# Optimization experiments

Hardware: AMD Instinct MI355X
Metric: run time of the kernel (lower is better)

The kernel has to match this reference:

```python
import jax, jax.numpy as jnp
import numpy as np
import math

B, Q, C, H, L, P = 8, 900, 256, 8, 4, 4
D = C // H  # head_dim = 32
SPATIAL = np.array([[100, 100], [50, 50], [25, 25], [13, 13]], dtype=np.int64)
AREAS = SPATIAL[:, 0] * SPATIAL[:, 1]
STARTS = np.concatenate([[0], np.cumsum(AREAS)[:-1]]).astype(np.int64)
S = int(AREAS.sum())  # 13294


def _xavier(k, i, o, scale=1.0):
    return jax.random.normal(k, (i, o), jnp.float32) * scale * (2.0 / (i + o)) ** 0.5


def setup_inputs() -> dict:
    key = jax.random.key(0)
    ks = jax.random.split(key, 16)
    inp = {}
    inp['query'] = jax.random.normal(ks[0], (B, Q, C), jnp.float32)
    inp['reference_points'] = jax.random.uniform(ks[1], (B, Q, L, 2), jnp.float32)
    inp['input_flatten'] = jax.random.normal(ks[2], (B, S, C), jnp.float32)
    inp['object_shape'] = jax.random.uniform(ks[3], (B, Q, 2), jnp.float32) * 0.3 + 0.02
    inp['input_spatial_shapes'] = jnp.asarray(SPATIAL)
    inp['input_level_start_index'] = jnp.asarray(STARTS)
    # learned parameters (torch zero-inits offset/attn weights; use small random for a nontrivial baseline)
    inp['w_q'] = _xavier(ks[4], C, C); inp['b_q'] = jnp.zeros((C,), jnp.float32)
    inp['w_v'] = _xavier(ks[5], C, C); inp['b_v'] = jnp.zeros((C,), jnp.float32)
    inp['w_o'] = _xavier(ks[6], C, C); inp['b_o'] = jnp.zeros((C,), jnp.float32)
    inp['w_off1'] = _xavier(ks[7], C + 2, C); inp['b_off1'] = jnp.zeros((C,), jnp.float32)
    inp['w_off2'] = _xavier(ks[8], C, H * L * P * 2, scale=0.05)
    inp['b_off2'] = jax.random.normal(ks[9], (H * L * P * 2,), jnp.float32) * 0.02
    inp['w_ax'] = _xavier(ks[10], C, H * L * P, scale=0.1); inp['b_ax'] = jnp.zeros((H * L * P,), jnp.float32)
    inp['w_ay'] = _xavier(ks[11], C, H * L * P, scale=0.1); inp['b_ay'] = jnp.zeros((H * L * P,), jnp.float32)
    # spectral basis per original init: head h uses freq pi*(h+1)/H over arange(D)
    freq = (np.arange(1, H + 1, dtype=np.float32)[:, None] * math.pi / H) * np.arange(D, dtype=np.float32)[None, :]
    inp['basis_x'] = jnp.asarray(np.cos(freq), jnp.float32)
    inp['basis_y'] = jnp.asarray(np.sin(freq), jnp.float32)
    return inp


def _bilinear_sample(v, locs):
    """v: (B,S,H,D); locs: (B,Q,H,L,P,2) in [0,1]. grid_sample semantics: align_corners=False, zeros padding.
    Returns (B,Q,H,L,P,D)."""
    levels = []
    for lvl in range(L):
        Hl, Wl = int(SPATIAL[lvl, 0]), int(SPATIAL[lvl, 1])
        start = int(STARTS[lvl])
        v_l = v[:, start:start + Hl * Wl]  # (B, Hl*Wl, H, D)
        loc = locs[:, :, :, lvl]  # (B,Q,H,P,2)
        # align_corners=False: pixel coord = loc * size - 0.5
        x = loc[..., 0] * Wl - 0.5
        y = loc[..., 1] * Hl - 0.5
        x0 = jnp.floor(x); y0 = jnp.floor(y)
        fx = x - x0; fy = y - y0
        x0i = x0.astype(jnp.int32); y0i = y0.astype(jnp.int32)
        acc = jnp.zeros((B, Q, H, P, D), jnp.float32)
        corners = [(0, 0, (1 - fx) * (1 - fy)), (1, 0, fx * (1 - fy)),
                   (0, 1, (1 - fx) * fy), (1, 1, fx * fy)]
        for dx, dy, w in corners:
            xi = x0i + dx; yi = y0i + dy
            valid = (xi >= 0) & (xi < Wl) & (yi >= 0) & (yi < Hl)
            idx = jnp.clip(yi, 0, Hl - 1) * Wl + jnp.clip(xi, 0, Wl - 1)  # (B,Q,H,P)
            idx_t = idx.transpose(0, 1, 3, 2).reshape(B, Q * P, H)[..., None]  # (B,Q*P,H,1)
            g = jnp.take_along_axis(v_l, idx_t, axis=1)  # (B,Q*P,H,D)
            g = g.reshape(B, Q, P, H, D).transpose(0, 1, 3, 2, 4)  # (B,Q,H,P,D)
            acc = acc + g * (w * valid.astype(jnp.float32))[..., None]
        levels.append(acc)
    return jnp.stack(levels, axis=3)  # (B,Q,H,L,P,D)


def reference(query, reference_points, input_flatten, input_spatial_shapes, input_level_start_index,
              object_shape, w_q, b_q, w_v, b_v, w_o, b_o, w_off1, b_off1, w_off2, b_off2,
              w_ax, b_ax, w_ay, b_ay, basis_x, basis_y):
    q = query @ w_q + b_q  # (B,Q,C)
    v = (input_flatten @ w_v + b_v).reshape(B, S, H, D)
    q_shape = jnp.concatenate([q, object_shape], axis=-1)  # (B,Q,C+2)
    hid = jax.nn.relu(q_shape @ w_off1 + b_off1)
    offsets = (hid @ w_off2 + b_off2).reshape(B, Q, H, L, P, 2)
    offsets = offsets * object_shape[:, :, None, None, None, :]
    ref = reference_points[:, :, None, :, None, :]  # (B,Q,1,L,1,2)
    locs = jnp.clip(ref + offsets, 0.0, 1.0)  # (B,Q,H,L,P,2)
    q_heads = q.reshape(B, Q, H, D)
    spec = jnp.einsum('bqhd,hd->bqh', q_heads, basis_x) * jnp.einsum('bqhd,hd->bqh', q_heads, basis_y)
    attn_x = (q @ w_ax + b_ax).reshape(B, Q, H, L, P)
    attn_y = (q @ w_ay + b_ay).reshape(B, Q, H, L, P)
    attn = attn_x * attn_y + spec[..., None, None]
    attn = jax.nn.softmax(attn.reshape(B, Q, H, L * P), axis=-1).reshape(B, Q, H, L, P)
    sampled = _bilinear_sample(v, locs)  # (B,Q,H,L,P,D)
    out = (sampled * attn[..., None]).sum(axis=(3, 4)).reshape(B, Q, C)
    return out @ w_o + b_o  # dropout is identity in eval
```

## Files before the change

kernel.cpp:

```cpp
#include <hip/hip_runtime.h>
#include <hip/hip_bf16.h>
#include <math.h>

constexpr int B_ = 8, Q_ = 900;
constexpr int S_ = 13294;
constexpr int BQ = 7200;
constexpr int BS = 106352;
constexpr int NVB = 831;

typedef __bf16 bf16x8 __attribute__((ext_vector_type(8)));
typedef float  f32x4  __attribute__((ext_vector_type(4)));

#define WAITLGKM0 asm volatile("s_waitcnt lgkmcnt(0)" ::: "memory")
#define SCHEDB    __builtin_amdgcn_sched_barrier(0)
#define BAR       __builtin_amdgcn_s_barrier()
#define CFENCE    asm volatile("" ::: "memory")

__device__ __forceinline__ void load_lds16(const void* g, void* lds) {
    __builtin_amdgcn_global_load_lds(
        (const __attribute__((address_space(1))) void*)g,
        (__attribute__((address_space(3))) void*)lds, 16, 0, 0);
}

__global__ __launch_bounds__(256)
void transpose_all(const float* __restrict__ wv, const float* __restrict__ wo,
                   const float* __restrict__ woff1, const float* __restrict__ woff2,
                   const float* __restrict__ wax, const float* __restrict__ way,
                   __bf16* __restrict__ tv, __bf16* __restrict__ to_,
                   __bf16* __restrict__ toff2, __bf16* __restrict__ tcat)
{
    const int bi = blockIdx.x;
    __shared__ float tile[32][33];
    const int tx = threadIdx.x & 31, ty = threadIdx.x >> 5;

    const float* src; __bf16* dst; int k0, n0, scol, sN = 256;
    if (bi < 192) {
        const int wid = bi >> 6, t = bi & 63;
        k0 = (t & 7) * 32; n0 = (t >> 3) * 32; scol = n0;
        if      (wid == 0) { src = wv;    dst = tv;    }
        else if (wid == 1) { src = wo;    dst = to_;   }
        else               { src = woff2; dst = toff2; }
    } else {
        const int t = bi - 192;
        k0 = (t & 7) * 32; n0 = (t >> 3) * 32;
        dst = tcat;
        if      (n0 < 128) { src = wax;   scol = n0;       sN = 128; }
        else if (n0 < 256) { src = way;   scol = n0 - 128; sN = 128; }
        else               { src = woff1; scol = n0 - 256; sN = 256; }
    }

    #pragma unroll
    for (int i = 0; i < 4; ++i)
        tile[ty + 8 * i][tx] = src[(size_t)(k0 + ty + 8 * i) * sN + scol + tx];
    __syncthreads();
    #pragma unroll
    for (int i = 0; i < 4; ++i)
        dst[(size_t)(n0 + ty + 8 * i) * 256 + k0 + tx] = (__bf16)tile[tx][ty + 8 * i];
}

__global__ __launch_bounds__(256)
void combine2(const __bf16* __restrict__ tcat, const float* __restrict__ wq,
              const float* __restrict__ bq, const float* __restrict__ bax,
              const float* __restrict__ bay, const float* __restrict__ boff1,
              __bf16* __restrict__ wcomb, float* __restrict__ bcomb)
{
    const int bi = blockIdx.x;
    if (bi >= 8) {
        const int n = (bi - 8) * 256 + threadIdx.x;
        float acc = (n < 128) ? bax[n] : (n < 256 ? bay[n - 128] : boff1[n - 256]);
        const __bf16* row = tcat + (size_t)n * 256;
        #pragma unroll 4
        for (int c8 = 0; c8 < 32; ++c8) {
            const bf16x8 rv = *(const bf16x8*)(row + c8 * 8);
            #pragma unroll
            for (int j = 0; j < 8; ++j) acc += bq[c8 * 8 + j] * (float)rv[j];
        }
        bcomb[n] = acc;
        return;
    }

    const int wid  = (bi << 2) + (threadIdx.x >> 6);
    const int lane = threadIdx.x & 63;
    const int n0 = (wid >> 2) * 64, k0 = (wid & 3) * 64;
    const int l15 = lane & 15, l4 = lane >> 4;

    f32x4 acc[4][4] = {};
    #pragma unroll
    for (int s = 0; s < 8; ++s) {
        const int c0 = s * 32 + l4 * 8;
        bf16x8 am[4], bm[4];
        #pragma unroll
        for (int mi = 0; mi < 4; ++mi)
            am[mi] = *(const bf16x8*)(tcat + (size_t)(n0 + mi * 16 + l15) * 256 + c0);
        #pragma unroll
        for (int ni = 0; ni < 4; ++ni) {
            const float* wr_ = wq + (size_t)(k0 + ni * 16 + l15) * 256 + c0;
            const float4 f0 = ((const float4*)wr_)[0];
            const float4 f1 = ((const float4*)wr_)[1];
            bm[ni][0] = (__bf16)f0.x; bm[ni][1] = (__bf16)f0.y;
            bm[ni][2] = (__bf16)f0.z; bm[ni][3] = (__bf16)f0.w;
            bm[ni][4] = (__bf16)f1.x; bm[ni][5] = (__bf16)f1.y;
            bm[ni][6] = (__bf16)f1.z; bm[ni][7] = (__bf16)f1.w;
        }
        #pragma unroll
        for (int mi = 0; mi < 4; ++mi)
            #pragma unroll
            for (int ni = 0; ni < 4; ++ni)
                acc[mi][ni] = __builtin_amdgcn_mfma_f32_16x16x32_bf16(
                    am[mi], bm[ni], acc[mi][ni], 0, 0, 0);
    }
    #pragma unroll
    for (int mi = 0; mi < 4; ++mi)
        #pragma unroll
        for (int rr = 0; rr < 4; ++rr) {
            const int n = n0 + mi * 16 + l4 * 4 + rr;
            #pragma unroll
            for (int ni = 0; ni < 4; ++ni)
                wcomb[(size_t)n * 256 + k0 + ni * 16 + l15] = (__bf16)acc[mi][ni][rr];
        }
}

__global__ __launch_bounds__(512)
void main_fused(const float* __restrict__ x_in, const __bf16* __restrict__ wt_v,
                const float* __restrict__ b_v, __bf16* __restrict__ v_bf,
                const float* __restrict__ query, const __bf16* __restrict__ wcomb,
                const float* __restrict__ bcomb, const float* __restrict__ objs,
                const float* __restrict__ wex, float* __restrict__ axyhid)
{
    __shared__ float4 AsbV[2][512];
    __shared__ float4 BsbV[3][1024];
    char* const Asb_b = (char*)AsbV;
    char* const Bsb_b = (char*)BsbV;

    const int bid  = blockIdx.x;
    const bool isV = (bid < NVB);
    const int qb   = bid - NVB;
    const int colhalf = isV ? 0 : (qb & 1);

    const float*  A    = isV ? x_in : query;
    const __bf16* Wt   = isV ? wt_v : (wcomb + (size_t)colhalf * 256 * 256);
    const float*  bias = isV ? b_v  : (bcomb + colhalf * 256);
    const int     M    = isV ? BS   : BQ;
    const int     row0 = isV ? bid * 128 : (qb >> 1) * 128;

    const int tid  = threadIdx.x;
    const int wave = tid >> 6, lane = tid & 63;
    const int wr = wave >> 2, wc = wave & 3;
    const int l15 = lane & 15, l4 = lane >> 4;

    const int st_row = tid >> 2, st_kq = tid & 3;
    const int gr_cl  = min(row0 + st_row, M - 1);
    const float* Abase = A + (size_t)gr_cl * 256 + st_kq * 8;
    const int a_wo = st_row * 64 + ((st_kq ^ ((st_row >> 1) & 3)) * 16);

    int a_off[4], b_off[4];
    #pragma unroll
    for (int mi = 0; mi < 4; ++mi) {
        const int r = wr * 64 + mi * 16 + l15;
        a_off[mi] = r * 64 + (l4 ^ ((r >> 1) & 3)) * 16;
    }
    #pragma unroll
    for (int ni = 0; ni < 4; ++ni) {
        const int c = wc * 64 + ni * 16 + l15;
        b_off[ni] = c * 64 + (l4 ^ ((c >> 1) & 3)) * 16;
    }

    const __bf16* bsrc[2];
    #pragma unroll
    for (int i = 0; i < 2; ++i) {
        const int c   = (wave * 2 + i) * 64 + lane;
        const int col = c >> 2, kcp = c & 3;
        const int kc  = kcp ^ ((col >> 1) & 3);
        bsrc[i] = Wt + (size_t)col * 256 + kc * 8;
    }

    auto issueB = [&](int kt, int bbuf) {
        #pragma unroll
        for (int i = 0; i < 2; ++i)
            load_lds16(bsrc[i] + kt * 32, Bsb_b + bbuf * 16384 + (wave * 2 + i) * 1024);
    };
    auto loadA = [&](int kt, float4* g) {
        const float* ga = Abase + kt * 32;
        g[0] = ((const float4*)ga)[0];
        g[1] = ((const float4*)ga)[1];
    };
    auto writeA = [&](int abuf, const float4* g) {
        bf16x8 c0;
        c0[0] = (__bf16)g[0].x; c0[1] = (__bf16)g[0].y; c0[2] = (__bf16)g[0].z; c0[3] = (__bf16)g[0].w;
        c0[4] = (__bf16)g[1].x; c0[5] = (__bf16)g[1].y; c0[6] = (__bf16)g[1].z; c0[7] = (__bf16)g[1].w;
        *(bf16x8*)(Asb_b + abuf * 8192 + a_wo) = c0;
    };

    f32x4 acc[4][4] = {};
    float4 g[2][2];

    issueB(0, 0);
    loadA(0, g[0]);
    issueB(1, 1);
    loadA(1, g[1]);
    writeA(0, g[0]);
    WAITLGKM0; BAR; CFENCE; SCHEDB;

    #pragma unroll
    for (int u = 0; u < 8; ++u) {
        if (u + 2 <= 7) {
            loadA(u + 2, g[u & 1]);
            issueB(u + 2, (u + 2) % 3);
        }

        const char* Ab = Asb_b + (u & 1) * 8192;
        const char* Bb = Bsb_b + (u % 3) * 16384;
        bf16x8 a[4], b[4];
        #pragma unroll
        for (int mi = 0; mi < 4; ++mi) a[mi] = *(const bf16x8*)(Ab + a_off[mi]);
        #pragma unroll
        for (int ni = 0; ni < 4; ++ni) b[ni] = *(const bf16x8*)(Bb + b_off[ni]);

        #pragma unroll
        for (int mi = 0; mi < 4; ++mi)
            #pragma unroll
            for (int ni = 0; ni < 4; ++ni)
                acc[mi][ni] = __builtin_amdgcn_mfma_f32_16x16x32_bf16(
                    a[mi], b[ni], acc[mi][ni], 0, 0, 0);

        if (u + 1 <= 7) {
            writeA((u + 1) & 1, g[(u + 1) & 1]);
            WAITLGKM0; BAR; CFENCE; SCHEDB;
        }
    }

    float bb[4];
    #pragma unroll
    for (int ni = 0; ni < 4; ++ni) bb[ni] = bias[wc * 64 + ni * 16 + l15];

    if (isV) {
        #pragma unroll
        for (int mi = 0; mi < 4; ++mi)
            #pragma unroll
            for (int rr = 0; rr < 4; ++rr) {
                const int row = row0 + wr * 64 + mi * 16 + l4 * 4 + rr;
                if (row >= M) continue;
                #pragma unroll
                for (int ni = 0; ni < 4; ++ni)
                    v_bf[(size_t)row * 256 + wc * 64 + ni * 16 + l15] =
                        (__bf16)(acc[mi][ni][rr] + bb[ni]);
            }
    } else {
        float we0[4], we1[4];
        #pragma unroll
        for (int ni = 0; ni < 4; ++ni) {
            const int c = wc * 64 + ni * 16 + l15;
            we0[ni] = colhalf ? wex[c]       : 0.f;
            we1[ni] = colhalf ? wex[256 + c] : 0.f;
        }
        #pragma unroll
        for (int mi = 0; mi < 4; ++mi)
            #pragma unroll
            for (int rr = 0; rr < 4; ++rr) {
                const int row = row0 + wr * 64 + mi * 16 + l4 * 4 + rr;
                if (row >= M) continue;
                const float e0 = objs[(size_t)row * 2];
                const float e1 = objs[(size_t)row * 2 + 1];
                #pragma unroll
                for (int ni = 0; ni < 4; ++ni) {
                    const int c = wc * 64 + ni * 16 + l15;
                    float v = acc[mi][ni][rr] + bb[ni];
                    if (colhalf) {
                        v += e0 * we0[ni] + e1 * we1[ni];
                        v = fmaxf(v, 0.f);
                    }
                    axyhid[(size_t)row * 512 + colhalf * 256 + c] = v;
                }
            }
    }
}

template<bool OUTBF16>
__global__ __launch_bounds__(256)
void gemm_dp(const float* __restrict__ A, const __bf16* __restrict__ Wt,
             const float* __restrict__ bias, void* __restrict__ outp,
             int M, int N, int LDA)
{
    __shared__ float4 AsbV[2][512];
    __shared__ float4 BsbV[3][512];
    char* const Asb_b = (char*)AsbV;
    char* const Bsb_b = (char*)BsbV;

    const int tid  = threadIdx.x;
    const int wave = tid >> 6, lane = tid & 63;
    const int wr = wave >> 1, wc = wave & 1;
    const int row0 = blockIdx.y * 128, col0 = blockIdx.x * 128;
    const int l15 = lane & 15, l4 = lane >> 4;

    const int st_row = tid >> 1, st_kh = tid & 1;
    const int gr_cl  = min(row0 + st_row, M - 1);
    const float* Abase = A + (size_t)gr_cl * LDA + st_kh * 16;
    const int asw   = (st_row >> 1) & 3;
    const int a_wo0 = st_row * 64 + ((st_kh * 2)     ^ asw) * 16;
    const int a_wo1 = st_row * 64 + ((st_kh * 2 + 1) ^ asw) * 16;

    int a_off[4], b_off[4];
    #pragma unroll
    for (int mi = 0; mi < 4; ++mi) {
        const int r   = wr * 64 + mi * 16 + l15;
        a_off[mi] = r * 64 + (l4 ^ ((r >> 1) & 3)) * 16;
    }
    #pragma unroll
    for (int ni = 0; ni < 4; ++ni) {
        const int c   = wc * 64 + ni * 16 + l15;
        b_off[ni] = c * 64 + (l4 ^ ((c >> 1) & 3)) * 16;
    }

    const __bf16* bsrc[2];
    #pragma unroll
    for (int i = 0; i < 2; ++i) {
        const int c   = (wave * 2 + i) * 64 + lane;
        const int col = c >> 2, kcp = c & 3;
        const int kc  = kcp ^ ((col >> 1) & 3);
        bsrc[i] = Wt + (size_t)(col0 + col) * 256 + kc * 8;
    }

    auto issueB = [&](int kt, int bbuf) {
        #pragma unroll
        for (int i = 0; i < 2; ++i)
            load_lds16(bsrc[i] + kt * 32, Bsb_b + bbuf * 8192 + (wave * 2 + i) * 1024);
    };
    auto loadA = [&](int kt, float4* g) {
        const float* ga = Abase + kt * 32;
        g[0] = ((const float4*)ga)[0];
        g[1] = ((const float4*)ga)[1];
        g[2] = ((const float4*)ga)[2];
        g[3] = ((const float4*)ga)[3];
    };
    auto writeA = [&](int abuf, const float4* g) {
        bf16x8 c0, c1;
        c0[0] = (__bf16)g[0].x; c0[1] = (__bf16)g[0].y; c0[2] = (__bf16)g[0].z; c0[3] = (__bf16)g[0].w;
        c0[4] = (__bf16)g[1].x; c0[5] = (__bf16)g[1].y; c0[6] = (__bf16)g[1].z; c0[7] = (__bf16)g[1].w;
        c1[0] = (__bf16)g[2].x; c1[1] = (__bf16)g[2].y; c1[2] = (__bf16)g[2].z; c1[3] = (__bf16)g[2].w;
        c1[4] = (__bf16)g[3].x; c1[5] = (__bf16)g[3].y; c1[6] = (__bf16)g[3].z; c1[7] = (__bf16)g[3].w;
        *(bf16x8*)(Asb_b + abuf * 8192 + a_wo0) = c0;
        *(bf16x8*)(Asb_b + abuf * 8192 + a_wo1) = c1;
    };

    f32x4 acc[4][4] = {};
    float4 g[2][4];

    issueB(0, 0);
    loadA(0, g[0]);
    issueB(1, 1);
    loadA(1, g[1]);
    writeA(0, g[0]);
    WAITLGKM0; BAR; CFENCE; SCHEDB;

    #pragma unroll
    for (int u = 0; u < 8; ++u) {
        if (u + 2 <= 7) {
            loadA(u + 2, g[u & 1]);
            issueB(u + 2, (u + 2) % 3);
        }

        const char* Ab = Asb_b + (u & 1) * 8192;
        const char* Bb = Bsb_b + (u % 3) * 8192;
        bf16x8 a[4], b[4];
        #pragma unroll
        for (int mi = 0; mi < 4; ++mi) a[mi] = *(const bf16x8*)(Ab + a_off[mi]);
        #pragma unroll
        for (int ni = 0; ni < 4; ++ni) b[ni] = *(const bf16x8*)(Bb + b_off[ni]);

        #pragma unroll
        for (int mi = 0; mi < 4; ++mi)
            #pragma unroll
            for (int ni = 0; ni < 4; ++ni)
                acc[mi][ni] = __builtin_amdgcn_mfma_f32_16x16x32_bf16(
                    a[mi], b[ni], acc[mi][ni], 0, 0, 0);

        if (u + 1 <= 7) {
            writeA((u + 1) & 1, g[(u + 1) & 1]);
            WAITLGKM0; BAR; CFENCE; SCHEDB;
        }
    }

    float bb[4];
    #pragma unroll
    for (int ni = 0; ni < 4; ++ni) bb[ni] = bias[col0 + wc * 64 + ni * 16 + l15];
    #pragma unroll
    for (int mi = 0; mi < 4; ++mi) {
        #pragma unroll
        for (int rr = 0; rr < 4; ++rr) {
            const int row = row0 + wr * 64 + mi * 16 + l4 * 4 + rr;
            if (row >= M) continue;
            #pragma unroll
            for (int ni = 0; ni < 4; ++ni) {
                const float v = acc[mi][ni][rr] + bb[ni];
                const int colb = col0 + wc * 64 + ni * 16 + l15;
                if (OUTBF16) ((__bf16*)outp)[(size_t)row * N + colb] = (__bf16)v;
                else         ((float*)outp)[(size_t)row * N + colb]  = v;
            }
        }
    }
}

__global__ __launch_bounds__(256)
void attn_sample_kernel(const float* __restrict__ axyhid,
                        const float* __restrict__ refp, const float* __restrict__ objs,
                        const float* __restrict__ off, const __bf16* __restrict__ v,
                        float* __restrict__ agg)
{
    const int bq = blockIdx.x;
    const int b  = bq / Q_;
    const int tid = threadIdx.x;

    __shared__ float sm[128];
    __shared__ float sa[128];
    __shared__ float sl[256];

    if (tid < 128)
        sm[tid] = axyhid[(size_t)bq * 512 + tid] * axyhid[(size_t)bq * 512 + 128 + tid];
    __syncthreads();

    if (tid < 128) {
        const int hh = tid >> 4;
        float mx = -1e30f;
        #pragma unroll
        for (int i = 0; i < 16; ++i) mx = fmaxf(mx, sm[hh * 16 + i]);
        float s = 0.f;
        #pragma unroll
        for (int i = 0; i < 16; ++i) s += __expf(sm[hh * 16 + i] - mx);
        sa[tid] = __expf(sm[tid] - mx) / s;

        const int l = (tid >> 2) & 3;
        const float os0 = objs[(size_t)bq * 2], os1 = objs[(size_t)bq * 2 + 1];
        const float r0 = refp[((size_t)bq * 4 + l) * 2];
        const float r1 = refp[((size_t)bq * 4 + l) * 2 + 1];
        const float o0 = off[(size_t)bq * 256 + tid * 2]     * os0;
        const float o1 = off[(size_t)bq * 256 + tid * 2 + 1] * os1;
        sl[tid * 2]     = fminf(fmaxf(r0 + o0, 0.f), 1.f);
        sl[tid * 2 + 1] = fminf(fmaxf(r1 + o1, 0.f), 1.f);
    }
    __syncthreads();

    const int h = tid >> 5, lane32 = tid & 31;
    const int sp = lane32 >> 2, cq = lane32 & 3;
    const int chbase = h * 32 + cq * 8;
    const __bf16* vb = v + (size_t)b * S_ * 256;

    float acc8[8] = {};

    #pragma unroll
    for (int gidx = 0; gidx < 2; ++gidx) {
        const int lp  = gidx * 8 + sp;
        const int li  = h * 16 + lp;
        const int lvl = lp >> 2;
        const int Wl = (lvl == 0) ? 100 : (lvl == 1) ? 50 : (lvl == 2) ? 25 : 13;
        const int Hl = Wl;
        const int st = (lvl == 0) ? 0 : (lvl == 1) ? 10000 : (lvl == 2) ? 12500 : 13125;

        const float a  = sa[li];
        const float lx = sl[li * 2], ly = sl[li * 2 + 1];
        const float x = lx * (float)Wl - 0.5f;
        const float y = ly * (float)Hl - 0.5f;
        const float x0f = floorf(x), y0f = floorf(y);
        const float fx = x - x0f, fy = y - y0f;
        const int x0 = (int)x0f, y0 = (int)y0f;

        #pragma unroll
        for (int c = 0; c < 4; ++c) {
            const int dx = c & 1, dy = c >> 1;
            const int xi = x0 + dx, yi = y0 + dy;
            const float wgt = (dx ? fx : 1.f - fx) * (dy ? fy : 1.f - fy);
            const bool valid = (xi >= 0) & (xi < Wl) & (yi >= 0) & (yi < Hl);
            const int idx = min(max(yi, 0), Hl - 1) * Wl + min(max(xi, 0), Wl - 1);
            const float wa = valid ? a * wgt : 0.f;
            const bf16x8 gv = *(const bf16x8*)(vb + (size_t)(st + idx) * 256 + chbase);
            #pragma unroll
            for (int j = 0; j < 8; ++j) acc8[j] += wa * (float)gv[j];
        }
    }

    #pragma unroll
    for (int m = 4; m <= 16; m <<= 1)
        #pragma unroll
        for (int j = 0; j < 8; ++j)
            acc8[j] += __shfl_xor(acc8[j], m);

    if (sp == 0) {
        #pragma unroll
        for (int j = 0; j < 8; ++j)
            agg[(size_t)bq * 256 + chbase + j] = acc8[j];
    }
}

extern "C" void kernel_launch(void* const* d_in, const int* in_sizes, int n_in,
                              void* d_out, int out_size, void* d_ws, size_t ws_size,
                              hipStream_t stream)
{
    const float* query = (const float*)d_in[0];
    const float* refp  = (const float*)d_in[1];
    const float* x_in  = (const float*)d_in[2];
    const float* objs  = (const float*)d_in[3];
    const float* w_q    = (const float*)d_in[6];
    const float* b_q    = (const float*)d_in[7];
    const float* w_v    = (const float*)d_in[8];
    const float* b_v    = (const float*)d_in[9];
    const float* w_o    = (const float*)d_in[10];
    const float* b_o    = (const float*)d_in[11];
    const float* w_off1 = (const float*)d_in[12];
    const float* b_off1 = (const float*)d_in[13];
    const float* w_off2 = (const float*)d_in[14];
    const float* b_off2 = (const float*)d_in[15];
    const float* w_ax   = (const float*)d_in[16];
    const float* b_ax   = (const float*)d_in[17];
    const float* w_ay   = (const float*)d_in[18];
    const float* b_ay   = (const float*)d_in[19];

    float* ws = (float*)d_ws;
    float* axyhid_ws = ws;
    float* off_ws    = axyhid_ws + (size_t)BQ * 512;
    float* agg_ws    = off_ws    + (size_t)BQ * 256;
    float* bcomb_ws  = agg_ws    + (size_t)BQ * 256;
    __bf16* v_bf    = (__bf16*)(bcomb_ws + 512);
    __bf16* wt_v    = v_bf    + (size_t)BS * 256;
    __bf16* wt_o    = wt_v    + 256 * 256;
    __bf16* wt_off2 = wt_o    + 256 * 256;
    __bf16* wt_cat  = wt_off2 + 256 * 256;
    __bf16* wcomb   = wt_cat  + 512 * 256;

    const dim3 blk(256);

    transpose_all<<<320, blk, 0, stream>>>(w_v, w_o, w_off1, w_off2, w_ax, w_ay,
                                           wt_v, wt_o, wt_off2, wt_cat);
    combine2<<<10, blk, 0, stream>>>(wt_cat, w_q, b_q, b_ax, b_ay, b_off1,
                                     wcomb, bcomb_ws);

    main_fused<<<NVB + 114, dim3(512), 0, stream>>>(
        x_in, wt_v, b_v, v_bf,
        query, wcomb, bcomb_ws, objs, w_off1 + 256 * 256, axyhid_ws);

    gemm_dp<false><<<dim3(2, (BQ + 127) / 128), blk, 0, stream>>>(
        axyhid_ws + 256, wt_off2, b_off2, off_ws, BQ, 256, 512);

    attn_sample_kernel<<<BQ, blk, 0, stream>>>(axyhid_ws, refp, objs, off_ws,
                                               v_bf, agg_ws);

    gemm_dp<false><<<dim3(2, (BQ + 127) / 128), blk, 0, stream>>>(
        agg_ws, wt_o, b_o, (float*)d_out, BQ, 256, 256);
}
```

Baseline: 106.6 us.

## Fuse offset GEMM, deformable sampling and output projection into one kernel

```diff
diff --git a/kernel.cpp b/kernel.cpp
--- a/kernel.cpp
+++ b/kernel.cpp
@@ -275,218 +275,195 @@
     }
 }
 
-template<bool OUTBF16>
 __global__ __launch_bounds__(256)
-void gemm_dp(const float* __restrict__ A, const __bf16* __restrict__ Wt,
-             const float* __restrict__ bias, void* __restrict__ outp,
-             int M, int N, int LDA)
+void mega_tail(const float* __restrict__ axyhid, const __bf16* __restrict__ wt_off2,
+               const float* __restrict__ b_off2, const float* __restrict__ refp,
+               const float* __restrict__ objs, const __bf16* __restrict__ v,
+               const __bf16* __restrict__ wt_o, const float* __restrict__ b_o,
+               float* __restrict__ outp)
 {
-    __shared__ float4 AsbV[2][512];
-    __shared__ float4 BsbV[3][512];
-    char* const Asb_b = (char*)AsbV;
-    char* const Bsb_b = (char*)BsbV;
-
-    const int tid  = threadIdx.x;
+    __shared__ float off_s[32][256];
+    __shared__ float sm_s[32][128];
+    __shared__ float sa_s[32][128];
+    __shared__ float sl_s[32][256];
+    __shared__ float agg_s[32][260];
+
+    const int bq0 = blockIdx.x * 32;
+    const int tid = threadIdx.x;
     const int wave = tid >> 6, lane = tid & 63;
-    const int wr = wave >> 1, wc = wave & 1;
-    const int row0 = blockIdx.y * 128, col0 = blockIdx.x * 128;
     const int l15 = lane & 15, l4 = lane >> 4;
 
-    const int st_row = tid >> 1, st_kh = tid & 1;
-    const int gr_cl  = min(row0 + st_row, M - 1);
-    const float* Abase = A + (size_t)gr_cl * LDA + st_kh * 16;
-    const int asw   = (st_row >> 1) & 3;
-    const int a_wo0 = st_row * 64 + ((st_kh * 2)     ^ asw) * 16;
-    const int a_wo1 = st_row * 64 + ((st_kh * 2 + 1) ^ asw) * 16;
-
-    int a_off[4], b_off[4];
-    #pragma unroll
-    for (int mi = 0; mi < 4; ++mi) {
-        const int r   = wr * 64 + mi * 16 + l15;
-        a_off[mi] = r * 64 + (l4 ^ ((r >> 1) & 3)) * 16;
-    }
-    #pragma unroll
-    for (int ni = 0; ni < 4; ++ni) {
-        const int c   = wc * 64 + ni * 16 + l15;
-        b_off[ni] = c * 64 + (l4 ^ ((c >> 1) & 3)) * 16;
-    }
-
-    const __bf16* bsrc[2];
-    #pragma unroll
-    for (int i = 0; i < 2; ++i) {
-        const int c   = (wave * 2 + i) * 64 + lane;
-        const int col = c >> 2, kcp = c & 3;
-        const int kc  = kcp ^ ((col >> 1) & 3);
-        bsrc[i] = Wt + (size_t)(col0 + col) * 256 + kc * 8;
-    }
-
-    auto issueB = [&](int kt, int bbuf) {
-        #pragma unroll
-        for (int i = 0; i < 2; ++i)
-            load_lds16(bsrc[i] + kt * 32, Bsb_b + bbuf * 8192 + (wave * 2 + i) * 1024);
-    };
-    auto loadA = [&](int kt, float4* g) {
-        const float* ga = Abase + kt * 32;
-        g[0] = ((const float4*)ga)[0];
-        g[1] = ((const float4*)ga)[1];
-        g[2] = ((const float4*)ga)[2];
-        g[3] = ((const float4*)ga)[3];
-    };
-    auto writeA = [&](int abuf, const float4* g) {
-        bf16x8 c0, c1;
-        c0[0] = (__bf16)g[0].x; c0[1] = (__bf16)g[0].y; c0[2] = (__bf16)g[0].z; c0[3] = (__bf16)g[0].w;
-        c0[4] = (__bf16)g[1].x; c0[5] = (__bf16)g[1].y; c0[6] = (__bf16)g[1].z; c0[7] = (__bf16)g[1].w;
-        c1[0] = (__bf16)g[2].x; c1[1] = (__bf16)g[2].y; c1[2] = (__bf16)g[2].z; c1[3] = (__bf16)g[2].w;
-        c1[4] = (__bf16)g[3].x; c1[5] = (__bf16)g[3].y; c1[6] = (__bf16)g[3].z; c1[7] = (__bf16)g[3].w;
-        *(bf16x8*)(Asb_b + abuf * 8192 + a_wo0) = c0;
-        *(bf16x8*)(Asb_b + abuf * 8192 + a_wo1) = c1;
-    };
-
-    f32x4 acc[4][4] = {};
-    float4 g[2][4];
-
-    issueB(0, 0);
-    loadA(0, g[0]);
-    issueB(1, 1);
-    loadA(1, g[1]);
-    writeA(0, g[0]);
-    WAITLGKM0; BAR; CFENCE; SCHEDB;
-
-    #pragma unroll
-    for (int u = 0; u < 8; ++u) {
-        if (u + 2 <= 7) {
-            loadA(u + 2, g[u & 1]);
-            issueB(u + 2, (u + 2) % 3);
-        }
-
-        const char* Ab = Asb_b + (u & 1) * 8192;
-        const char* Bb = Bsb_b + (u % 3) * 8192;
-        bf16x8 a[4], b[4];
-        #pragma unroll
-        for (int mi = 0; mi < 4; ++mi) a[mi] = *(const bf16x8*)(Ab + a_off[mi]);
-        #pragma unroll
-        for (int ni = 0; ni < 4; ++ni) b[ni] = *(const bf16x8*)(Bb + b_off[ni]);
-
-        #pragma unroll
-        for (int mi = 0; mi < 4; ++mi)
+    {
+        f32x4 acc[2][4] = {};
+        #pragma unroll
+        for (int kt = 0; kt < 8; ++kt) {
+            const int k0 = kt * 32 + l4 * 8;
+            bf16x8 am[2], bm[4];
+            #pragma unroll
+            for (int mi = 0; mi < 2; ++mi) {
+                const float* ap = axyhid + (size_t)(bq0 + mi * 16 + l15) * 512 + 256 + k0;
+                const float4 f0 = ((const float4*)ap)[0];
+                const float4 f1 = ((const float4*)ap)[1];
+                am[mi][0] = (__bf16)f0.x; am[mi][1] = (__bf16)f0.y;
+                am[mi][2] = (__bf16)f0.z; am[mi][3] = (__bf16)f0.w;
+                am[mi][4] = (__bf16)f1.x; am[mi][5] = (__bf16)f1.y;
+                am[mi][6] = (__bf16)f1.z; am[mi][7] = (__bf16)f1.w;
+            }
             #pragma unroll
             for (int ni = 0; ni < 4; ++ni)
-                acc[mi][ni] = __builtin_amdgcn_mfma_f32_16x16x32_bf16(
-                    a[mi], b[ni], acc[mi][ni], 0, 0, 0);
-
-        if (u + 1 <= 7) {
-            writeA((u + 1) & 1, g[(u + 1) & 1]);
-            WAITLGKM0; BAR; CFENCE; SCHEDB;
-        }
-    }
-
-    float bb[4];
-    #pragma unroll
-    for (int ni = 0; ni < 4; ++ni) bb[ni] = bias[col0 + wc * 64 + ni * 16 + l15];
-    #pragma unroll
-    for (int mi = 0; mi < 4; ++mi) {
-        #pragma unroll
-        for (int rr = 0; rr < 4; ++rr) {
-            const int row = row0 + wr * 64 + mi * 16 + l4 * 4 + rr;
-            if (row >= M) continue;
-            #pragma unroll
-            for (int ni = 0; ni < 4; ++ni) {
-                const float v = acc[mi][ni][rr] + bb[ni];
-                const int colb = col0 + wc * 64 + ni * 16 + l15;
-                if (OUTBF16) ((__bf16*)outp)[(size_t)row * N + colb] = (__bf16)v;
-                else         ((float*)outp)[(size_t)row * N + colb]  = v;
-            }
-        }
-    }
-}
-
-__global__ __launch_bounds__(256)
-void attn_sample_kernel(const float* __restrict__ axyhid,
-                        const float* __restrict__ refp, const float* __restrict__ objs,
-                        const float* __restrict__ off, const __bf16* __restrict__ v,
-                        float* __restrict__ agg)
-{
-    const int bq = blockIdx.x;
-    const int b  = bq / Q_;
-    const int tid = threadIdx.x;
-
-    __shared__ float sm[128];
-    __shared__ float sa[128];
-    __shared__ float sl[256];
-
-    if (tid < 128)
-        sm[tid] = axyhid[(size_t)bq * 512 + tid] * axyhid[(size_t)bq * 512 + 128 + tid];
+                bm[ni] = *(const bf16x8*)(wt_off2 + (size_t)(wave * 64 + ni * 16 + l15) * 256 + k0);
+            #pragma unroll
+            for (int mi = 0; mi < 2; ++mi)
+                #pragma unroll
+                for (int ni = 0; ni < 4; ++ni)
+                    acc[mi][ni] = __builtin_amdgcn_mfma_f32_16x16x32_bf16(
+                        am[mi], bm[ni], acc[mi][ni], 0, 0, 0);
+        }
+        #pragma unroll
+        for (int mi = 0; mi < 2; ++mi)
+            #pragma unroll
+            for (int rr = 0; rr < 4; ++rr) {
+                const int r = mi * 16 + l4 * 4 + rr;
+                #pragma unroll
+                for (int ni = 0; ni < 4; ++ni) {
+                    const int c = wave * 64 + ni * 16 + l15;
+                    off_s[r][c] = acc[mi][ni][rr] + b_off2[c];
+                }
+            }
+    }
     __syncthreads();
 
-    if (tid < 128) {
-        const int hh = tid >> 4;
+    #pragma unroll
+    for (int it = 0; it < 16; ++it) {
+        const int idx = it * 256 + tid;
+        const int r = idx >> 7, u = idx & 127;
+        const int bq = bq0 + r;
+        sm_s[r][u] = axyhid[(size_t)bq * 512 + u] * axyhid[(size_t)bq * 512 + 128 + u];
+    }
+    __syncthreads();
+    #pragma unroll
+    for (int it = 0; it < 16; ++it) {
+        const int idx = it * 256 + tid;
+        const int r = idx >> 7, u = idx & 127;
+        const int bq = bq0 + r;
+        const int hh = u >> 4;
         float mx = -1e30f;
         #pragma unroll
-        for (int i = 0; i < 16; ++i) mx = fmaxf(mx, sm[hh * 16 + i]);
+        for (int i = 0; i < 16; ++i) mx = fmaxf(mx, sm_s[r][hh * 16 + i]);
         float s = 0.f;
         #pragma unroll
-        for (int i = 0; i < 16; ++i) s += __expf(sm[hh * 16 + i] - mx);
-        sa[tid] = __expf(sm[tid] - mx) / s;
-
-        const int l = (tid >> 2) & 3;
+        for (int i = 0; i < 16; ++i) s += __expf(sm_s[r][hh * 16 + i] - mx);
+        sa_s[r][u] = __expf(sm_s[r][u] - mx) / s;
+
+        const int l = (u >> 2) & 3;
         const float os0 = objs[(size_t)bq * 2], os1 = objs[(size_t)bq * 2 + 1];
         const float r0 = refp[((size_t)bq * 4 + l) * 2];
         const float r1 = refp[((size_t)bq * 4 + l) * 2 + 1];
-        const float o0 = off[(size_t)bq * 256 + tid * 2]     * os0;
-        const float o1 = off[(size_t)bq * 256 + tid * 2 + 1] * os1;
-        sl[tid * 2]     = fminf(fmaxf(r0 + o0, 0.f), 1.f);
-        sl[tid * 2 + 1] = fminf(fmaxf(r1 + o1, 0.f), 1.f);
+        const float o0 = off_s[r][u * 2]     * os0;
+        const float o1 = off_s[r][u * 2 + 1] * os1;
+        sl_s[r][u * 2]     = fminf(fmaxf(r0 + o0, 0.f), 1.f);
+        sl_s[r][u * 2 + 1] = fminf(fmaxf(r1 + o1, 0.f), 1.f);
     }
     __syncthreads();
 
     const int h = tid >> 5, lane32 = tid & 31;
     const int sp = lane32 >> 2, cq = lane32 & 3;
     const int chbase = h * 32 + cq * 8;
-    const __bf16* vb = v + (size_t)b * S_ * 256;
-
-    float acc8[8] = {};
-
-    #pragma unroll
-    for (int gidx = 0; gidx < 2; ++gidx) {
-        const int lp  = gidx * 8 + sp;
-        const int li  = h * 16 + lp;
-        const int lvl = lp >> 2;
-        const int Wl = (lvl == 0) ? 100 : (lvl == 1) ? 50 : (lvl == 2) ? 25 : 13;
-        const int Hl = Wl;
-        const int st = (lvl == 0) ? 0 : (lvl == 1) ? 10000 : (lvl == 2) ? 12500 : 13125;
-
-        const float a  = sa[li];
-        const float lx = sl[li * 2], ly = sl[li * 2 + 1];
-        const float x = lx * (float)Wl - 0.5f;
-        const float y = ly * (float)Hl - 0.5f;
-        const float x0f = floorf(x), y0f = floorf(y);
-        const float fx = x - x0f, fy = y - y0f;
-        const int x0 = (int)x0f, y0 = (int)y0f;
-
-        #pragma unroll
-        for (int c = 0; c < 4; ++c) {
-            const int dx = c & 1, dy = c >> 1;
-            const int xi = x0 + dx, yi = y0 + dy;
-            const float wgt = (dx ? fx : 1.f - fx) * (dy ? fy : 1.f - fy);
-            const bool valid = (xi >= 0) & (xi < Wl) & (yi >= 0) & (yi < Hl);
-            const int idx = min(max(yi, 0), Hl - 1) * Wl + min(max(xi, 0), Wl - 1);
-            const float wa = valid ? a * wgt : 0.f;
-            const bf16x8 gv = *(const bf16x8*)(vb + (size_t)(st + idx) * 256 + chbase);
-            #pragma unroll
-            for (int j = 0; j < 8; ++j) acc8[j] += wa * (float)gv[j];
-        }
-    }
-
-    #pragma unroll
-    for (int m = 4; m <= 16; m <<= 1)
-        #pragma unroll
-        for (int j = 0; j < 8; ++j)
-            acc8[j] += __shfl_xor(acc8[j], m);
-
-    if (sp == 0) {
-        #pragma unroll
-        for (int j = 0; j < 8; ++j)
-            agg[(size_t)bq * 256 + chbase + j] = acc8[j];
+
+    auto sample_row = [&](int r, float* acc8) {
+        const int bq = bq0 + r;
+        const __bf16* vb = v + (size_t)(bq / Q_) * S_ * 256;
+        #pragma unroll
+        for (int gidx = 0; gidx < 2; ++gidx) {
+            const int lp  = gidx * 8 + sp;
+            const int li  = h * 16 + lp;
+            const int lvl = lp >> 2;
+            const int Wl = (lvl == 0) ? 100 : (lvl == 1) ? 50 : (lvl == 2) ? 25 : 13;
+            const int Hl = Wl;
+            const int st = (lvl == 0) ? 0 : (lvl == 1) ? 10000 : (lvl == 2) ? 12500 : 13125;
+
+            const float a  = sa_s[r][li];
+            const float lx = sl_s[r][li * 2], ly = sl_s[r][li * 2 + 1];
+            const float x = lx * (float)Wl - 0.5f;
+            const float y = ly * (float)Hl - 0.5f;
+            const float x0f = floorf(x), y0f = floorf(y);
+            const float fx = x - x0f, fy = y - y0f;
+            const int x0 = (int)x0f, y0 = (int)y0f;
+
+            #pragma unroll
+            for (int c = 0; c < 4; ++c) {
+                const int dx = c & 1, dy = c >> 1;
+                const int xi = x0 + dx, yi = y0 + dy;
+                const float wgt = (dx ? fx : 1.f - fx) * (dy ? fy : 1.f - fy);
+                const bool valid = (xi >= 0) & (xi < Wl) & (yi >= 0) & (yi < Hl);
+                const int idx = min(max(yi, 0), Hl - 1) * Wl + min(max(xi, 0), Wl - 1);
+                const float wa = valid ? a * wgt : 0.f;
+                const bf16x8 gv = *(const bf16x8*)(vb + (size_t)(st + idx) * 256 + chbase);
+                #pragma unroll
+                for (int j = 0; j < 8; ++j) acc8[j] += wa * (float)gv[j];
+            }
+        }
+    };
+
+    #pragma unroll 2
+    for (int r2 = 0; r2 < 32; r2 += 2) {
+        float accA[8] = {}, accB[8] = {};
+        sample_row(r2,     accA);
+        sample_row(r2 + 1, accB);
+        #pragma unroll
+        for (int m = 4; m <= 16; m <<= 1)
+            #pragma unroll
+            for (int j = 0; j < 8; ++j) {
+                accA[j] += __shfl_xor(accA[j], m);
+                accB[j] += __shfl_xor(accB[j], m);
+            }
+        if (sp == 0) {
+            #pragma unroll
+            for (int j = 0; j < 8; ++j) {
+                agg_s[r2][chbase + j]     = accA[j];
+                agg_s[r2 + 1][chbase + j] = accB[j];
+            }
+        }
+    }
+    __syncthreads();
+
+    {
+        f32x4 acc[2][4] = {};
+        #pragma unroll
+        for (int kt = 0; kt < 8; ++kt) {
+            const int k0 = kt * 32 + l4 * 8;
+            bf16x8 am[2], bm[4];
+            #pragma unroll
+            for (int mi = 0; mi < 2; ++mi) {
+                const float* ap = &agg_s[mi * 16 + l15][k0];
+                const float4 f0 = ((const float4*)ap)[0];
+                const float4 f1 = ((const float4*)ap)[1];
+                am[mi][0] = (__bf16)f0.x; am[mi][1] = (__bf16)f0.y;
+                am[mi][2] = (__bf16)f0.z; am[mi][3] = (__bf16)f0.w;
+                am[mi][4] = (__bf16)f1.x; am[mi][5] = (__bf16)f1.y;
+                am[mi][6] = (__bf16)f1.z; am[mi][7] = (__bf16)f1.w;
+            }
+            #pragma unroll
+            for (int ni = 0; ni < 4; ++ni)
+                bm[ni] = *(const bf16x8*)(wt_o + (size_t)(wave * 64 + ni * 16 + l15) * 256 + k0);
+            #pragma unroll
+            for (int mi = 0; mi < 2; ++mi)
+                #pragma unroll
+                for (int ni = 0; ni < 4; ++ni)
+                    acc[mi][ni] = __builtin_amdgcn_mfma_f32_16x16x32_bf16(
+                        am[mi], bm[ni], acc[mi][ni], 0, 0, 0);
+        }
+        #pragma unroll
+        for (int mi = 0; mi < 2; ++mi)
+            #pragma unroll
+            for (int rr = 0; rr < 4; ++rr) {
+                const int row = bq0 + mi * 16 + l4 * 4 + rr;
+                #pragma unroll
+                for (int ni = 0; ni < 4; ++ni) {
+                    const int c = wave * 64 + ni * 16 + l15;
+                    outp[(size_t)row * 256 + c] = acc[mi][ni][rr] + b_o[c];
+                }
+            }
     }
 }
 
@@ -515,9 +492,7 @@
 
     float* ws = (float*)d_ws;
     float* axyhid_ws = ws;
-    float* off_ws    = axyhid_ws + (size_t)BQ * 512;
-    float* agg_ws    = off_ws    + (size_t)BQ * 256;
-    float* bcomb_ws  = agg_ws    + (size_t)BQ * 256;
+    float* bcomb_ws  = axyhid_ws + (size_t)BQ * 512;
     __bf16* v_bf    = (__bf16*)(bcomb_ws + 512);
     __bf16* wt_v    = v_bf    + (size_t)BS * 256;
     __bf16* wt_o    = wt_v    + 256 * 256;
@@ -536,12 +511,6 @@
         x_in, wt_v, b_v, v_bf,
         query, wcomb, bcomb_ws, objs, w_off1 + 256 * 256, axyhid_ws);
 
-    gemm_dp<false><<<dim3(2, (BQ + 127) / 128), blk, 0, stream>>>(
-        axyhid_ws + 256, wt_off2, b_off2, off_ws, BQ, 256, 512);
-
-    attn_sample_kernel<<<BQ, blk, 0, stream>>>(axyhid_ws, refp, objs, off_ws,
-                                               v_bf, agg_ws);
-
-    gemm_dp<false><<<dim3(2, (BQ + 127) / 128), blk, 0, stream>>>(
-        agg_ws, wt_o, b_o, (float*)d_out, BQ, 256, 256);
+    mega_tail<<<BQ / 32, blk, 0, stream>>>(
+        axyhid_ws, wt_off2, b_off2, refp, objs, v_bf, wt_o, b_o, (float*)d_out);
 }
```

After: 115.9 us. 8.7% more time.

## Read GEMM weight operand directly from global memory instead of LDS staging

Applied to the files above, without the earlier changes.

```diff
diff --git a/kernel.cpp b/kernel.cpp
--- a/kernel.cpp
+++ b/kernel.cpp
@@ -128,9 +128,7 @@
                 const float* __restrict__ wex, float* __restrict__ axyhid)
 {
     __shared__ float4 AsbV[2][512];
-    __shared__ float4 BsbV[3][1024];
     char* const Asb_b = (char*)AsbV;
-    char* const Bsb_b = (char*)BsbV;
 
     const int bid  = blockIdx.x;
     const bool isV = (bid < NVB);
@@ -153,32 +151,18 @@
     const float* Abase = A + (size_t)gr_cl * 256 + st_kq * 8;
     const int a_wo = st_row * 64 + ((st_kq ^ ((st_row >> 1) & 3)) * 16);
 
-    int a_off[4], b_off[4];
+    int a_off[4];
     #pragma unroll
     for (int mi = 0; mi < 4; ++mi) {
         const int r = wr * 64 + mi * 16 + l15;
         a_off[mi] = r * 64 + (l4 ^ ((r >> 1) & 3)) * 16;
     }
-    #pragma unroll
-    for (int ni = 0; ni < 4; ++ni) {
-        const int c = wc * 64 + ni * 16 + l15;
-        b_off[ni] = c * 64 + (l4 ^ ((c >> 1) & 3)) * 16;
-    }
-
-    const __bf16* bsrc[2];
-    #pragma unroll
-    for (int i = 0; i < 2; ++i) {
-        const int c   = (wave * 2 + i) * 64 + lane;
-        const int col = c >> 2, kcp = c & 3;
-        const int kc  = kcp ^ ((col >> 1) & 3);
-        bsrc[i] = Wt + (size_t)col * 256 + kc * 8;
-    }
-
-    auto issueB = [&](int kt, int bbuf) {
-        #pragma unroll
-        for (int i = 0; i < 2; ++i)
-            load_lds16(bsrc[i] + kt * 32, Bsb_b + bbuf * 16384 + (wave * 2 + i) * 1024);
-    };
+
+    const __bf16* bp[4];
+    #pragma unroll
+    for (int ni = 0; ni < 4; ++ni)
+        bp[ni] = Wt + (size_t)(wc * 64 + ni * 16 + l15) * 256 + l4 * 8;
+
     auto loadA = [&](int kt, float4* g) {
         const float* ga = Abase + kt * 32;
         g[0] = ((const float4*)ga)[0];
@@ -192,29 +176,24 @@
     };
 
     f32x4 acc[4][4] = {};
-    float4 g[2][2];
-
-    issueB(0, 0);
-    loadA(0, g[0]);
-    issueB(1, 1);
-    loadA(1, g[1]);
-    writeA(0, g[0]);
-    WAITLGKM0; BAR; CFENCE; SCHEDB;
+    float4 g[2];
+
+    loadA(0, g);
+    writeA(0, g);
 
     #pragma unroll
     for (int u = 0; u < 8; ++u) {
-        if (u + 2 <= 7) {
-            loadA(u + 2, g[u & 1]);
-            issueB(u + 2, (u + 2) % 3);
-        }
+        if (u < 7) loadA(u + 1, g);
+        WAITLGKM0; BAR; CFENCE; SCHEDB;
 
         const char* Ab = Asb_b + (u & 1) * 8192;
-        const char* Bb = Bsb_b + (u % 3) * 16384;
         bf16x8 a[4], b[4];
         #pragma unroll
         for (int mi = 0; mi < 4; ++mi) a[mi] = *(const bf16x8*)(Ab + a_off[mi]);
         #pragma unroll
-        for (int ni = 0; ni < 4; ++ni) b[ni] = *(const bf16x8*)(Bb + b_off[ni]);
+        for (int ni = 0; ni < 4; ++ni) b[ni] = *(const bf16x8*)(bp[ni] + u * 32);
+
+        if (u < 7) writeA((u + 1) & 1, g);
 
         #pragma unroll
         for (int mi = 0; mi < 4; ++mi)
@@ -222,11 +201,6 @@
             for (int ni = 0; ni < 4; ++ni)
                 acc[mi][ni] = __builtin_amdgcn_mfma_f32_16x16x32_bf16(
                     a[mi], b[ni], acc[mi][ni], 0, 0, 0);
-
-        if (u + 1 <= 7) {
-            writeA((u + 1) & 1, g[(u + 1) & 1]);
-            WAITLGKM0; BAR; CFENCE; SCHEDB;
-        }
     }
 
     float bb[4];
```

After: 112.5 us. 1.06x slower.

## Merge weight transpose and combine kernels into one prep launch; add explicit vmcnt waits

Applied to the files above, without the earlier changes.

```diff
diff --git a/kernel.cpp b/kernel.cpp
--- a/kernel.cpp
+++ b/kernel.cpp
@@ -22,64 +22,58 @@
         (__attribute__((address_space(3))) void*)lds, 16, 0, 0);
 }
 
+__device__ __forceinline__ float wcat_f(const float* __restrict__ wax,
+                                        const float* __restrict__ way,
+                                        const float* __restrict__ woff1,
+                                        int c, int n)
+{
+    if (n < 128) return wax[(size_t)c * 128 + n];
+    if (n < 256) return way[(size_t)c * 128 + (n - 128)];
+    return woff1[(size_t)c * 256 + (n - 256)];
+}
+
 __global__ __launch_bounds__(256)
-void transpose_all(const float* __restrict__ wv, const float* __restrict__ wo,
-                   const float* __restrict__ woff1, const float* __restrict__ woff2,
-                   const float* __restrict__ wax, const float* __restrict__ way,
-                   __bf16* __restrict__ tv, __bf16* __restrict__ to_,
-                   __bf16* __restrict__ toff2, __bf16* __restrict__ tcat)
+void prep_all(const float* __restrict__ wv, const float* __restrict__ wo,
+              const float* __restrict__ woff2, const float* __restrict__ wq,
+              const float* __restrict__ wax, const float* __restrict__ way,
+              const float* __restrict__ woff1, const float* __restrict__ bq,
+              const float* __restrict__ bax, const float* __restrict__ bay,
+              const float* __restrict__ boff1,
+              __bf16* __restrict__ tv, __bf16* __restrict__ to_,
+              __bf16* __restrict__ toff2, __bf16* __restrict__ wcomb,
+              float* __restrict__ bcomb)
 {
     const int bi = blockIdx.x;
     __shared__ float tile[32][33];
-    const int tx = threadIdx.x & 31, ty = threadIdx.x >> 5;
-
-    const float* src; __bf16* dst; int k0, n0, scol, sN = 256;
+
     if (bi < 192) {
         const int wid = bi >> 6, t = bi & 63;
-        k0 = (t & 7) * 32; n0 = (t >> 3) * 32; scol = n0;
+        const int k0 = (t & 7) * 32, n0 = (t >> 3) * 32;
+        const int tx = threadIdx.x & 31, ty = threadIdx.x >> 5;
+        const float* src; __bf16* dst;
         if      (wid == 0) { src = wv;    dst = tv;    }
         else if (wid == 1) { src = wo;    dst = to_;   }
         else               { src = woff2; dst = toff2; }
-    } else {
-        const int t = bi - 192;
-        k0 = (t & 7) * 32; n0 = (t >> 3) * 32;
-        dst = tcat;
-        if      (n0 < 128) { src = wax;   scol = n0;       sN = 128; }
-        else if (n0 < 256) { src = way;   scol = n0 - 128; sN = 128; }
-        else               { src = woff1; scol = n0 - 256; sN = 256; }
-    }
-
-    #pragma unroll
-    for (int i = 0; i < 4; ++i)
-        tile[ty + 8 * i][tx] = src[(size_t)(k0 + ty + 8 * i) * sN + scol + tx];
-    __syncthreads();
-    #pragma unroll
-    for (int i = 0; i < 4; ++i)
-        dst[(size_t)(n0 + ty + 8 * i) * 256 + k0 + tx] = (__bf16)tile[tx][ty + 8 * i];
-}
-
-__global__ __launch_bounds__(256)
-void combine2(const __bf16* __restrict__ tcat, const float* __restrict__ wq,
-              const float* __restrict__ bq, const float* __restrict__ bax,
-              const float* __restrict__ bay, const float* __restrict__ boff1,
-              __bf16* __restrict__ wcomb, float* __restrict__ bcomb)
-{
-    const int bi = blockIdx.x;
-    if (bi >= 8) {
-        const int n = (bi - 8) * 256 + threadIdx.x;
+        #pragma unroll
+        for (int i = 0; i < 4; ++i)
+            tile[ty + 8 * i][tx] = src[(size_t)(k0 + ty + 8 * i) * 256 + n0 + tx];
+        __syncthreads();
+        #pragma unroll
+        for (int i = 0; i < 4; ++i)
+            dst[(size_t)(n0 + ty + 8 * i) * 256 + k0 + tx] = (__bf16)tile[tx][ty + 8 * i];
+        return;
+    }
+
+    if (bi >= 200) {
+        const int n = (bi - 200) * 256 + threadIdx.x;
         float acc = (n < 128) ? bax[n] : (n < 256 ? bay[n - 128] : boff1[n - 256]);
-        const __bf16* row = tcat + (size_t)n * 256;
-        #pragma unroll 4
-        for (int c8 = 0; c8 < 32; ++c8) {
-            const bf16x8 rv = *(const bf16x8*)(row + c8 * 8);
-            #pragma unroll
-            for (int j = 0; j < 8; ++j) acc += bq[c8 * 8 + j] * (float)rv[j];
-        }
+        for (int c = 0; c < 256; ++c)
+            acc += bq[c] * (float)(__bf16)wcat_f(wax, way, woff1, c, n);
         bcomb[n] = acc;
         return;
     }
 
-    const int wid  = (bi << 2) + (threadIdx.x >> 6);
+    const int wid  = ((bi - 192) << 2) + (threadIdx.x >> 6);
     const int lane = threadIdx.x & 63;
     const int n0 = (wid >> 2) * 64, k0 = (wid & 3) * 64;
     const int l15 = lane & 15, l4 = lane >> 4;
@@ -90,8 +84,12 @@
         const int c0 = s * 32 + l4 * 8;
         bf16x8 am[4], bm[4];
         #pragma unroll
-        for (int mi = 0; mi < 4; ++mi)
-            am[mi] = *(const bf16x8*)(tcat + (size_t)(n0 + mi * 16 + l15) * 256 + c0);
+        for (int mi = 0; mi < 4; ++mi) {
+            const int n = n0 + mi * 16 + l15;
+            #pragma unroll
+            for (int j = 0; j < 8; ++j)
+                am[mi][j] = (__bf16)wcat_f(wax, way, woff1, c0 + j, n);
+        }
         #pragma unroll
         for (int ni = 0; ni < 4; ++ni) {
             const float* wr_ = wq + (size_t)(k0 + ni * 16 + l15) * 256 + c0;
@@ -207,6 +205,11 @@
             loadA(u + 2, g[u & 1]);
             issueB(u + 2, (u + 2) % 3);
         }
+
+        if (u < 6)       { asm volatile("s_waitcnt vmcnt(8)" ::: "memory"); }
+        else if (u == 6) { asm volatile("s_waitcnt vmcnt(4)" ::: "memory"); }
+        else             { asm volatile("s_waitcnt vmcnt(0)" ::: "memory"); }
+        SCHEDB;
 
         const char* Ab = Asb_b + (u & 1) * 8192;
         const char* Bb = Bsb_b + (u % 3) * 16384;
@@ -358,6 +361,11 @@
             loadA(u + 2, g[u & 1]);
             issueB(u + 2, (u + 2) % 3);
         }
+
+        if (u < 6)       { asm volatile("s_waitcnt vmcnt(12)" ::: "memory"); }
+        else if (u == 6) { asm volatile("s_waitcnt vmcnt(6)" ::: "memory"); }
+        else             { asm volatile("s_waitcnt vmcnt(0)" ::: "memory"); }
+        SCHEDB;
 
         const char* Ab = Asb_b + (u & 1) * 8192;
         const char* Bb = Bsb_b + (u % 3) * 8192;
@@ -522,15 +530,13 @@
     __bf16* wt_v    = v_bf    + (size_t)BS * 256;
     __bf16* wt_o    = wt_v    + 256 * 256;
     __bf16* wt_off2 = wt_o    + 256 * 256;
-    __bf16* wt_cat  = wt_off2 + 256 * 256;
-    __bf16* wcomb   = wt_cat  + 512 * 256;
+    __bf16* wcomb   = wt_off2 + 256 * 256;
 
     const dim3 blk(256);
 
-    transpose_all<<<320, blk, 0, stream>>>(w_v, w_o, w_off1, w_off2, w_ax, w_ay,
-                                           wt_v, wt_o, wt_off2, wt_cat);
-    combine2<<<10, blk, 0, stream>>>(wt_cat, w_q, b_q, b_ax, b_ay, b_off1,
-                                     wcomb, bcomb_ws);
+    prep_all<<<202, blk, 0, stream>>>(w_v, w_o, w_off2, w_q, w_ax, w_ay, w_off1,
+                                      b_q, b_ax, b_ay, b_off1,
+                                      wt_v, wt_o, wt_off2, wcomb, bcomb_ws);
 
     main_fused<<<NVB + 114, dim3(512), 0, stream>>>(
         x_in, wt_v, b_v, v_bf,
```

Measured after the change: 108.9 us. 1.02x slower.
